# Performance work log

Measured on AMD Instinct MI355X. Metric: run time of the kernel, lower is better.

Reference implementation:

```python
import jax, jax.numpy as jnp
import numpy as np

B, S, H = 8, 2048, 1024
D = H // 16  # head_size = hidden_size // n_heads = 64


def setup_inputs() -> dict:
    key = jax.random.key(0)
    ks = jax.random.split(key, 7)
    scale = 1.0 / np.sqrt(H)
    x = jax.random.normal(ks[0], (B, S, H), dtype=jnp.float32)
    mask = jnp.ones((B, S), dtype=jnp.int32)
    Wq = jax.random.uniform(ks[1], (H, D), jnp.float32, -scale, scale)
    bq = jax.random.uniform(ks[2], (D,), jnp.float32, -scale, scale)
    Wk = jax.random.uniform(ks[3], (H, D), jnp.float32, -scale, scale)
    bk = jax.random.uniform(ks[4], (D,), jnp.float32, -scale, scale)
    Wv = jax.random.uniform(ks[5], (H, D), jnp.float32, -scale, scale)
    bv = jax.random.uniform(ks[6], (D,), jnp.float32, -scale, scale)
    return {"x": x, "mask": mask, "Wq": Wq, "bq": bq, "Wk": Wk, "bk": bk, "Wv": Wv, "bv": bv}


def reference(x, mask, Wq, bq, Wk, bk, Wv, bv):
    # projections: [B,S,H] @ [H,D] -> [B,S,D]
    q = jnp.einsum("bsh,hd->bsd", x, Wq) + bq
    k = jnp.einsum("bsh,hd->bsd", x, Wk) + bk
    v = jnp.einsum("bsh,hd->bsd", x, Wv) + bv
    # scores: [B,S,S]
    scores = jnp.einsum("bqd,bkd->bqk", q, k) / jnp.sqrt(jnp.asarray(q.shape[-1], q.dtype))
    # mask: [B,S] -> [B,1,S]; fill masked keys with -inf
    scores = jnp.where(mask[:, None, :] == 0, -jnp.inf, scores)
    attn = jax.nn.softmax(scores, axis=-1)
    # dropout prob is 0.0 (inference semantics) -> identity
    return jnp.einsum("bqk,bkd->bqd", attn, v)
```

## Files before the change

### kernel.cpp

```cpp
#include <hip/hip_runtime.h>

typedef __bf16 bf16x8 __attribute__((ext_vector_type(8)));
typedef __bf16 bf16x4 __attribute__((ext_vector_type(4)));
typedef float f32x4 __attribute__((ext_vector_type(4)));
typedef float f32x16 __attribute__((ext_vector_type(16)));
typedef unsigned short u16x8 __attribute__((ext_vector_type(8)));

#define MFMA16(a, b, c) __builtin_amdgcn_mfma_f32_16x16x32_bf16((a), (b), (c), 0, 0, 0)
#define MFMA32(a, b, c) __builtin_amdgcn_mfma_f32_32x32x16_bf16((a), (b), (c), 0, 0, 0)

#define SCALE_Q 0.180336880f
#define DEFER_TH 11.5415603f

static __device__ __forceinline__ float fexp2(float x) {
  return __builtin_amdgcn_exp2f(x);
}

static __device__ __forceinline__ unsigned short f2bf(float f) {
  unsigned int u = __float_as_uint(f);
  u += 0x7fffu + ((u >> 16) & 1u);
  return (unsigned short)(u >> 16);
}
static __device__ __forceinline__ float bf2f(unsigned short s) {
  return __uint_as_float((unsigned int)s << 16);
}
static __device__ __forceinline__ unsigned int cvtpk(float lo, float hi) {
  unsigned int r;
  asm("v_cvt_pk_bf16_f32 %0, %1, %2" : "=v"(r) : "v"(lo), "v"(hi));
  return r;
}
static __device__ __forceinline__ void plswap(unsigned int& a, unsigned int& b) {
  asm("v_permlane32_swap_b32 %0, %1" : "+v"(a), "+v"(b));
}

static __device__ __forceinline__ void gld_lds16(const void* g, void* l) {
  __builtin_amdgcn_global_load_lds(
      (const __attribute__((address_space(1))) unsigned int*)(g),
      (__attribute__((address_space(3))) unsigned int*)(l), 16, 0, 0);
}

__global__ __launch_bounds__(128) void wt_kernel(
    const float* __restrict__ Wq, const float* __restrict__ Wk,
    const float* __restrict__ Wv, unsigned short* __restrict__ Wt,
    const int* __restrict__ mask, float* __restrict__ mAddG) {
  const int bid = blockIdx.x;
  if (bid >= 192) {
    const int idx = (bid - 192) * 128 + threadIdx.x;
    mAddG[idx] = mask[idx] ? 0.0f : -__builtin_inff();
    return;
  }
  const int n = bid;
  const int jl = threadIdx.x;
  const float* W;
  int col;
  float scale;
  if (n < 64)       { W = Wq; col = n;       scale = SCALE_Q; }
  else if (n < 128) { W = Wk; col = n - 64;  scale = 1.0f; }
  else              { W = Wv; col = n - 128; scale = 1.0f; }
  const int js = (jl & ~7) | ((jl & 7) ^ (n & 7));
  u16x8 o;
#pragma unroll
  for (int e = 0; e < 8; ++e) o[e] = f2bf(W[(jl * 8 + e) * 64 + col] * scale);
  *reinterpret_cast<u16x8*>(&Wt[n * 1024 + js * 8]) = o;
}

__global__ __launch_bounds__(512, 4) void qkv_kernel(
    const float* __restrict__ x, const unsigned short* __restrict__ Wt,
    const float* __restrict__ bq, const float* __restrict__ bk,
    const float* __restrict__ bv, unsigned short* __restrict__ Q,
    unsigned short* __restrict__ K, unsigned short* __restrict__ Vt) {
  __shared__ __align__(16) unsigned short xs[2][32][72];
  __shared__ __align__(16) unsigned short ws[2][192 * 64];
  const int tid = threadIdx.x;
  const int w = tid >> 6, lane = tid & 63;
  const int lr = lane & 15, lg = lane >> 4;
  const int wg = w >> 2, wc = w & 3;
  const int m0 = blockIdx.x * 32;

  const int xrow = tid >> 4, xc4 = (tid & 15) * 4;
  const float* xsrc = x + (m0 + xrow) * 1024 + xc4;
  const unsigned short* wsrc0 = Wt + ((0 * 512 + tid) >> 3) * 1024 + (tid & 7) * 8;
  const unsigned short* wsrc1 = Wt + ((1 * 512 + tid) >> 3) * 1024 + (tid & 7) * 8;
  const unsigned short* wsrc2 = Wt + ((2 * 512 + tid) >> 3) * 1024 + (tid & 7) * 8;

  f32x4 acc[3] = {};
  const int arow = wg * 16 + lr;

#define WSTAGE(k0, buf)                                                      \
  do {                                                                       \
    gld_lds16(wsrc0 + (k0), (char*)(&ws[buf][0]) + w * 1024);                \
    gld_lds16(wsrc1 + (k0), (char*)(&ws[buf][0]) + 8192 + w * 1024);         \
    gld_lds16(wsrc2 + (k0), (char*)(&ws[buf][0]) + 16384 + w * 1024);        \
  } while (0)
#define XWRITE(v, buf)                                                       \
  do {                                                                       \
    bf16x4 xb;                                                               \
    xb[0] = (__bf16)(v).x; xb[1] = (__bf16)(v).y;                            \
    xb[2] = (__bf16)(v).z; xb[3] = (__bf16)(v).w;                            \
    *reinterpret_cast<bf16x4*>(&xs[buf][xrow][xc4]) = xb;                    \
  } while (0)

  float4 xrA = *reinterpret_cast<const float4*>(xsrc);
  WSTAGE(0, 0);
  XWRITE(xrA, 0);
  xrA = *reinterpret_cast<const float4*>(xsrc + 64);
  asm volatile("s_waitcnt vmcnt(1) lgkmcnt(0)" ::: "memory");
  __builtin_amdgcn_s_barrier();

#pragma unroll
  for (int t = 0; t < 16; ++t) {
    const int cur = t & 1;
    if (t < 15) WSTAGE((t + 1) * 64, cur ^ 1);
    __builtin_amdgcn_sched_barrier(0);
    float4 xrB = {};
    if (t < 14)
      xrB = *reinterpret_cast<const float4*>(xsrc + (t + 2) * 64);
    __builtin_amdgcn_sched_barrier(0);

    bf16x8 a[2];
#pragma unroll
    for (int kh = 0; kh < 2; ++kh)
      a[kh] = *reinterpret_cast<const bf16x8*>(&xs[cur][arow][kh * 32 + lg * 8]);
#pragma unroll
    for (int cf = 0; cf < 3; ++cf) {
      const int n = wc * 48 + cf * 16 + lr;
      const unsigned short* wr = &ws[cur][n * 64];
#pragma unroll
      for (int kh = 0; kh < 2; ++kh) {
        const int sc = (kh * 4 + lg) ^ (n & 7);
        bf16x8 bv8 = *reinterpret_cast<const bf16x8*>(wr + sc * 8);
        acc[cf] = MFMA16(a[kh], bv8, acc[cf]);
      }
    }
    if (t < 15) {
      XWRITE(xrA, cur ^ 1);
      if (t < 14)
        asm volatile("s_waitcnt vmcnt(1) lgkmcnt(0)" ::: "memory");
      else
        asm volatile("s_waitcnt vmcnt(0) lgkmcnt(0)" ::: "memory");
      __builtin_amdgcn_s_barrier();
      xrA = xrB;
    }
  }
#undef WSTAGE
#undef XWRITE

  const int mb = m0 + wg * 16 + lg * 4;
  const int b = m0 >> 11;
#pragma unroll
  for (int cf = 0; cf < 3; ++cf) {
    const int n = wc * 48 + cf * 16 + lr;
    if (n < 64) {
      const float bias = bq[n] * SCALE_Q;
#pragma unroll
      for (int i = 0; i < 4; ++i) Q[(mb + i) * 64 + n] = f2bf(acc[cf][i] + bias);
    } else if (n < 128) {
      const int nn = n - 64;
      const float bias = bk[nn];
#pragma unroll
      for (int i = 0; i < 4; ++i) K[(mb + i) * 64 + nn] = f2bf(acc[cf][i] + bias);
    } else {
      const int d = n - 128;
      const float bias = bv[d];
      ushort4 o;
      o.x = f2bf(acc[cf][0] + bias);
      o.y = f2bf(acc[cf][1] + bias);
      o.z = f2bf(acc[cf][2] + bias);
      o.w = f2bf(acc[cf][3] + bias);
      const int sl = (m0 & 2047) + wg * 16 + lg * 4;
      *reinterpret_cast<ushort4*>(&Vt[((b * 64 + d) << 11) + sl]) = o;
    }
  }
}

__global__ __launch_bounds__(256) void attn_kernel(
    const unsigned short* __restrict__ Q, const unsigned short* __restrict__ K,
    const unsigned short* __restrict__ Vt, const float* __restrict__ mAddG,
    const int* __restrict__ maskI, unsigned short* __restrict__ Opb,
    float* __restrict__ mp, float* __restrict__ lp) {
  __shared__ __align__(16) unsigned short ks[64][72];
  __shared__ __align__(16) unsigned short vs[64][72];
  __shared__ int fl[4];

  const int qt = blockIdx.x, b = blockIdx.y, c = blockIdx.z;
  const int tid = threadIdx.x;
  const int w = tid >> 6, lane = tid & 63;
  const int l31 = lane & 31, h = lane >> 5;
  const int bh = b * 2048;
  const int qb = qt * 128 + w * 32;
  const int sr = tid >> 3, scc = (tid & 7) * 8;

  {
    const int mz = ((maskI[bh + c * 512 + tid] == 0) ? 1 : 0) |
                   ((maskI[bh + c * 512 + 256 + tid] == 0) ? 1 : 0);
    const unsigned long long bal = __ballot(mz);
    if (lane == 0) fl[w] = (bal != 0ull) ? 1 : 0;
  }
  __syncthreads();
  const bool hasMask = (fl[0] | fl[1] | fl[2] | fl[3]) != 0;

  bf16x8 qf[4];
#pragma unroll
  for (int dt = 0; dt < 4; ++dt)
    qf[dt] = *reinterpret_cast<const bf16x8*>(
        &Q[(bh + qb + l31) * 64 + dt * 16 + h * 8]);

  uint4 rk0, rk1, rv0, rv1;
  {
    const int kv0 = c * 512;
    rk0 = *reinterpret_cast<const uint4*>(&K[(bh + kv0 + sr) * 64 + scc]);
    rk1 = *reinterpret_cast<const uint4*>(&K[(bh + kv0 + 32 + sr) * 64 + scc]);
    rv0 = *reinterpret_cast<const uint4*>(&Vt[(b * 64 + sr) * 2048 + kv0 + scc]);
    rv1 = *reinterpret_cast<const uint4*>(&Vt[(b * 64 + 32 + sr) * 2048 + kv0 + scc]);
  }

  f32x16 oacc[2] = {};
  float m_s = -__builtin_inff(), l_s = 0.0f;

  for (int it = 0; it < 8; ++it) {
    const int kv0 = c * 512 + it * 64;
    __builtin_amdgcn_s_barrier();

    *reinterpret_cast<uint4*>(&ks[sr][scc]) = rk0;
    *reinterpret_cast<uint4*>(&ks[32 + sr][scc]) = rk1;
    *reinterpret_cast<uint4*>(&vs[sr][scc]) = rv0;
    *reinterpret_cast<uint4*>(&vs[32 + sr][scc]) = rv1;

    if (it < 7) {
      const int kvn = kv0 + 64;
      rk0 = *reinterpret_cast<const uint4*>(&K[(bh + kvn + sr) * 64 + scc]);
      rk1 = *reinterpret_cast<const uint4*>(&K[(bh + kvn + 32 + sr) * 64 + scc]);
      rv0 = *reinterpret_cast<const uint4*>(&Vt[(b * 64 + sr) * 2048 + kvn + scc]);
      rv1 = *reinterpret_cast<const uint4*>(&Vt[(b * 64 + 32 + sr) * 2048 + kvn + scc]);
    }

    asm volatile("s_waitcnt lgkmcnt(0)" ::: "memory");
    __builtin_amdgcn_s_barrier();

    f32x16 st0 = {}, st1 = {};
    __builtin_amdgcn_s_setprio(1);
#pragma unroll
    for (int dt = 0; dt < 4; ++dt) {
      const bf16x8 kf0 = *reinterpret_cast<const bf16x8*>(&ks[l31][dt * 16 + h * 8]);
      st0 = MFMA32(kf0, qf[dt], st0);
    }
#pragma unroll
    for (int dt = 0; dt < 4; ++dt) {
      const bf16x8 kf1 = *reinterpret_cast<const bf16x8*>(&ks[32 + l31][dt * 16 + h * 8]);
      st1 = MFMA32(kf1, qf[dt], st1);
    }
    __builtin_amdgcn_s_setprio(0);

    if (hasMask) {
#pragma unroll
      for (int rb = 0; rb < 4; ++rb) {
        const f32x4 md0 =
            *reinterpret_cast<const f32x4*>(&mAddG[bh + kv0 + rb * 8 + 4 * h]);
        const f32x4 md1 = *reinterpret_cast<const f32x4*>(
            &mAddG[bh + kv0 + 32 + rb * 8 + 4 * h]);
#pragma unroll
        for (int j = 0; j < 4; ++j) {
          st0[rb * 4 + j] += md0[j];
          st1[rb * 4 + j] += md1[j];
        }
      }
    }

    float pm = st0[0];
#pragma unroll
    for (int r = 1; r < 16; ++r) pm = fmaxf(pm, st0[r]);
#pragma unroll
    for (int r = 0; r < 16; ++r) pm = fmaxf(pm, st1[r]);
    pm = fmaxf(pm, __shfl_xor(pm, 32));
    const float nm = fmaxf(m_s, pm);
    if (!__all(nm <= m_s + DEFER_TH)) {
      const float scn = fexp2(m_s - nm);
      m_s = nm;
      l_s *= scn;
#pragma unroll
      for (int r = 0; r < 16; ++r) {
        const float scr = __shfl(scn, (r & 3) + 8 * (r >> 2) + 4 * h);
        oacc[0][r] *= scr;
        oacc[1][r] *= scr;
      }
    }
    const float mexp = (m_s == -__builtin_inff()) ? 0.0f : m_s;
    float rs = 0.0f;
#pragma unroll
    for (int r = 0; r < 16; ++r) {
      const float p0 = fexp2(st0[r] - mexp);
      st0[r] = p0;
      rs += p0;
      const float p1 = fexp2(st1[r] - mexp);
      st1[r] = p1;
      rs += p1;
    }
    rs += __shfl_xor(rs, 32);
    l_s += rs;

    unsigned int paw[4][4];
#pragma unroll
    for (int kt16 = 0; kt16 < 4; ++kt16) {
      const int lo = kt16 & 1;
      unsigned int X0, X1, Y0, Y1;
      if (kt16 < 2) {
        X0 = cvtpk(st0[lo * 8 + 0], st0[lo * 8 + 1]);
        Y0 = cvtpk(st0[lo * 8 + 2], st0[lo * 8 + 3]);
        X1 = cvtpk(st0[lo * 8 + 4], st0[lo * 8 + 5]);
        Y1 = cvtpk(st0[lo * 8 + 6], st0[lo * 8 + 7]);
      } else {
        X0 = cvtpk(st1[lo * 8 + 0], st1[lo * 8 + 1]);
        Y0 = cvtpk(st1[lo * 8 + 2], st1[lo * 8 + 3]);
        X1 = cvtpk(st1[lo * 8 + 4], st1[lo * 8 + 5]);
        Y1 = cvtpk(st1[lo * 8 + 6], st1[lo * 8 + 7]);
      }
      plswap(X0, X1);
      plswap(Y0, Y1);
      paw[kt16][0] = X0;
      paw[kt16][1] = Y0;
      paw[kt16][2] = X1;
      paw[kt16][3] = Y1;
    }

    __builtin_amdgcn_s_setprio(1);
#pragma unroll
    for (int nf = 0; nf < 2; ++nf)
#pragma unroll
      for (int kt16 = 0; kt16 < 4; ++kt16) {
        const bf16x8 vb = *reinterpret_cast<const bf16x8*>(
            &vs[nf * 32 + l31][kt16 * 16 + h * 8]);
        const bf16x8 pa = *reinterpret_cast<const bf16x8*>(&paw[kt16][0]);
        oacc[nf] = MFMA32(pa, vb, oacc[nf]);
      }
    __builtin_amdgcn_s_setprio(0);
  }

  const float inv_s = (l_s > 0.0f) ? 1.0f / l_s : 0.0f;
#pragma unroll
  for (int r = 0; r < 16; ++r) {
    const int qoff = (r & 3) + 8 * (r >> 2) + 4 * h;
    const float invr = __shfl(inv_s, qoff);
    const int row = bh + qb + qoff;
    Opb[(c * 16384 + row) * 64 + l31] = f2bf(oacc[0][r] * invr);
    Opb[(c * 16384 + row) * 64 + 32 + l31] = f2bf(oacc[1][r] * invr);
  }
  if (h == 0) {
    mp[c * 16384 + bh + qb + l31] = m_s;
    lp[c * 16384 + bh + qb + l31] = l_s;
  }
}

__global__ __launch_bounds__(256) void merge_kernel(
    const unsigned short* __restrict__ Opb, const float* __restrict__ mp,
    const float* __restrict__ lp, float* __restrict__ out) {
  const int t = blockIdx.x * 256 + threadIdx.x;
  const int row = t >> 4;
  const int cc = (t & 15) * 4;
  float mv[4], lv[4];
#pragma unroll
  for (int c = 0; c < 4; ++c) {
    mv[c] = mp[c * 16384 + row];
    lv[c] = lp[c * 16384 + row];
  }
  float M = fmaxf(fmaxf(mv[0], mv[1]), fmaxf(mv[2], mv[3]));
  float L = 0.0f;
  f32x4 o = {};
#pragma unroll
  for (int c = 0; c < 4; ++c) {
    const float wc = __builtin_amdgcn_exp2f(mv[c] - M) * lv[c];
    L += wc;
    const ushort4 u = *reinterpret_cast<const ushort4*>(
        &Opb[(c * 16384 + row) * 64 + cc]);
    f32x4 oc;
    oc[0] = bf2f(u.x); oc[1] = bf2f(u.y); oc[2] = bf2f(u.z); oc[3] = bf2f(u.w);
    o += oc * wc;
  }
  const float inv = 1.0f / L;
  *reinterpret_cast<f32x4*>(&out[row * 64 + cc]) = o * inv;
}

extern "C" void kernel_launch(void* const* d_in, const int* in_sizes, int n_in,
                              void* d_out, int out_size, void* d_ws, size_t ws_size,
                              hipStream_t stream) {
  const float* x  = (const float*)d_in[0];
  const int* mask = (const int*)d_in[1];
  const float* Wq = (const float*)d_in[2];
  const float* bq = (const float*)d_in[3];
  const float* Wk = (const float*)d_in[4];
  const float* bk = (const float*)d_in[5];
  const float* Wv = (const float*)d_in[6];
  const float* bv = (const float*)d_in[7];
  float* out = (float*)d_out;

  unsigned short* Wt = (unsigned short*)d_ws;
  unsigned short* Qw = Wt + 192 * 1024;
  unsigned short* Kw = Qw + 16384 * 64;
  unsigned short* Vt = Kw + 16384 * 64;
  unsigned short* Opb = Vt + 16384 * 64;
  float* mAddG = (float*)(Opb + 4 * 16384 * 64);
  float* mp = mAddG + 16384;
  float* lp = mp + 4 * 16384;

  hipLaunchKernelGGL(wt_kernel, dim3(320), dim3(128), 0, stream,
                     Wq, Wk, Wv, Wt, mask, mAddG);
  hipLaunchKernelGGL(qkv_kernel, dim3(512), dim3(512), 0, stream,
                     x, Wt, bq, bk, bv, Qw, Kw, Vt);
  hipLaunchKernelGGL(attn_kernel, dim3(16, 8, 4), dim3(256), 0, stream,
                     Qw, Kw, Vt, mAddG, mask, Opb, mp, lp);
  hipLaunchKernelGGL(merge_kernel, dim3(1024), dim3(256), 0, stream,
                     Opb, mp, lp, out);
}
```

Before: 47.96 us.

## Double QKV projection M-tile to 64 rows to reuse weight tiles

The QKV projection kernel now processes 64 rows of x per block instead of 32. Each wave computes two 16-row sub-tiles, so every weight fragment read from LDS feeds two MFMAs, and the grid halves to 256 blocks. This cuts redundant weight loads from global memory and LDS per output row. In exchange it uses more accumulators and registers, lowers the occupancy hint to 2, and leaves fewer blocks than CUs on a 256-CU device, which may reduce parallelism.

```diff
diff --git a/kernel.cpp b/kernel.cpp
--- a/kernel.cpp
+++ b/kernel.cpp
@@ -64,18 +64,18 @@
   *reinterpret_cast<u16x8*>(&Wt[n * 1024 + js * 8]) = o;
 }
 
-__global__ __launch_bounds__(512, 4) void qkv_kernel(
+__global__ __launch_bounds__(512, 2) void qkv_kernel(
     const float* __restrict__ x, const unsigned short* __restrict__ Wt,
     const float* __restrict__ bq, const float* __restrict__ bk,
     const float* __restrict__ bv, unsigned short* __restrict__ Q,
     unsigned short* __restrict__ K, unsigned short* __restrict__ Vt) {
-  __shared__ __align__(16) unsigned short xs[2][32][72];
+  __shared__ __align__(16) unsigned short xs[2][64][72];
   __shared__ __align__(16) unsigned short ws[2][192 * 64];
   const int tid = threadIdx.x;
   const int w = tid >> 6, lane = tid & 63;
   const int lr = lane & 15, lg = lane >> 4;
   const int wg = w >> 2, wc = w & 3;
-  const int m0 = blockIdx.x * 32;
+  const int m0 = blockIdx.x * 64;
 
   const int xrow = tid >> 4, xc4 = (tid & 15) * 4;
   const float* xsrc = x + (m0 + xrow) * 1024 + xc4;
@@ -83,8 +83,8 @@
   const unsigned short* wsrc1 = Wt + ((1 * 512 + tid) >> 3) * 1024 + (tid & 7) * 8;
   const unsigned short* wsrc2 = Wt + ((2 * 512 + tid) >> 3) * 1024 + (tid & 7) * 8;
 
-  f32x4 acc[3] = {};
-  const int arow = wg * 16 + lr;
+  f32x4 acc[2][3] = {};
+  const int arow = wg * 32 + lr;
 
 #define WSTAGE(k0, buf)                                                      \
   do {                                                                       \
@@ -92,19 +92,24 @@
     gld_lds16(wsrc1 + (k0), (char*)(&ws[buf][0]) + 8192 + w * 1024);         \
     gld_lds16(wsrc2 + (k0), (char*)(&ws[buf][0]) + 16384 + w * 1024);        \
   } while (0)
-#define XWRITE(v, buf)                                                       \
+#define XWRITE(v0, v1, buf)                                                  \
   do {                                                                       \
-    bf16x4 xb;                                                               \
-    xb[0] = (__bf16)(v).x; xb[1] = (__bf16)(v).y;                            \
-    xb[2] = (__bf16)(v).z; xb[3] = (__bf16)(v).w;                            \
-    *reinterpret_cast<bf16x4*>(&xs[buf][xrow][xc4]) = xb;                    \
+    bf16x4 t0, t1;                                                           \
+    t0[0] = (__bf16)(v0).x; t0[1] = (__bf16)(v0).y;                          \
+    t0[2] = (__bf16)(v0).z; t0[3] = (__bf16)(v0).w;                          \
+    t1[0] = (__bf16)(v1).x; t1[1] = (__bf16)(v1).y;                          \
+    t1[2] = (__bf16)(v1).z; t1[3] = (__bf16)(v1).w;                          \
+    *reinterpret_cast<bf16x4*>(&xs[buf][xrow][xc4]) = t0;                    \
+    *reinterpret_cast<bf16x4*>(&xs[buf][xrow + 32][xc4]) = t1;               \
   } while (0)
 
-  float4 xrA = *reinterpret_cast<const float4*>(xsrc);
+  float4 xrA0 = *reinterpret_cast<const float4*>(xsrc);
+  float4 xrA1 = *reinterpret_cast<const float4*>(xsrc + 32 * 1024);
   WSTAGE(0, 0);
-  XWRITE(xrA, 0);
-  xrA = *reinterpret_cast<const float4*>(xsrc + 64);
-  asm volatile("s_waitcnt vmcnt(1) lgkmcnt(0)" ::: "memory");
+  XWRITE(xrA0, xrA1, 0);
+  xrA0 = *reinterpret_cast<const float4*>(xsrc + 64);
+  xrA1 = *reinterpret_cast<const float4*>(xsrc + 32 * 1024 + 64);
+  asm volatile("s_waitcnt vmcnt(2) lgkmcnt(0)" ::: "memory");
   __builtin_amdgcn_s_barrier();
 
 #pragma unroll
@@ -112,15 +117,20 @@
     const int cur = t & 1;
     if (t < 15) WSTAGE((t + 1) * 64, cur ^ 1);
     __builtin_amdgcn_sched_barrier(0);
-    float4 xrB = {};
-    if (t < 14)
-      xrB = *reinterpret_cast<const float4*>(xsrc + (t + 2) * 64);
+    float4 xrB0 = {}, xrB1 = {};
+    if (t < 14) {
+      xrB0 = *reinterpret_cast<const float4*>(xsrc + (t + 2) * 64);
+      xrB1 = *reinterpret_cast<const float4*>(xsrc + 32 * 1024 + (t + 2) * 64);
+    }
     __builtin_amdgcn_sched_barrier(0);
 
-    bf16x8 a[2];
-#pragma unroll
-    for (int kh = 0; kh < 2; ++kh)
-      a[kh] = *reinterpret_cast<const bf16x8*>(&xs[cur][arow][kh * 32 + lg * 8]);
+    bf16x8 a[2][2];
+#pragma unroll
+    for (int sub = 0; sub < 2; ++sub)
+#pragma unroll
+      for (int kh = 0; kh < 2; ++kh)
+        a[sub][kh] = *reinterpret_cast<const bf16x8*>(
+            &xs[cur][arow + sub * 16][kh * 32 + lg * 8]);
 #pragma unroll
     for (int cf = 0; cf < 3; ++cf) {
       const int n = wc * 48 + cf * 16 + lr;
@@ -128,47 +138,54 @@
 #pragma unroll
       for (int kh = 0; kh < 2; ++kh) {
         const int sc = (kh * 4 + lg) ^ (n & 7);
-        bf16x8 bv8 = *reinterpret_cast<const bf16x8*>(wr + sc * 8);
-        acc[cf] = MFMA16(a[kh], bv8, acc[cf]);
+        const bf16x8 bv8 = *reinterpret_cast<const bf16x8*>(wr + sc * 8);
+        acc[0][cf] = MFMA16(a[0][kh], bv8, acc[0][cf]);
+        acc[1][cf] = MFMA16(a[1][kh], bv8, acc[1][cf]);
       }
     }
     if (t < 15) {
-      XWRITE(xrA, cur ^ 1);
+      XWRITE(xrA0, xrA1, cur ^ 1);
       if (t < 14)
-        asm volatile("s_waitcnt vmcnt(1) lgkmcnt(0)" ::: "memory");
+        asm volatile("s_waitcnt vmcnt(2) lgkmcnt(0)" ::: "memory");
       else
         asm volatile("s_waitcnt vmcnt(0) lgkmcnt(0)" ::: "memory");
       __builtin_amdgcn_s_barrier();
-      xrA = xrB;
+      xrA0 = xrB0;
+      xrA1 = xrB1;
     }
   }
 #undef WSTAGE
 #undef XWRITE
 
-  const int mb = m0 + wg * 16 + lg * 4;
   const int b = m0 >> 11;
 #pragma unroll
-  for (int cf = 0; cf < 3; ++cf) {
-    const int n = wc * 48 + cf * 16 + lr;
-    if (n < 64) {
-      const float bias = bq[n] * SCALE_Q;
-#pragma unroll
-      for (int i = 0; i < 4; ++i) Q[(mb + i) * 64 + n] = f2bf(acc[cf][i] + bias);
-    } else if (n < 128) {
-      const int nn = n - 64;
-      const float bias = bk[nn];
-#pragma unroll
-      for (int i = 0; i < 4; ++i) K[(mb + i) * 64 + nn] = f2bf(acc[cf][i] + bias);
-    } else {
-      const int d = n - 128;
-      const float bias = bv[d];
-      ushort4 o;
-      o.x = f2bf(acc[cf][0] + bias);
-      o.y = f2bf(acc[cf][1] + bias);
-      o.z = f2bf(acc[cf][2] + bias);
-      o.w = f2bf(acc[cf][3] + bias);
-      const int sl = (m0 & 2047) + wg * 16 + lg * 4;
-      *reinterpret_cast<ushort4*>(&Vt[((b * 64 + d) << 11) + sl]) = o;
+  for (int sub = 0; sub < 2; ++sub) {
+    const int mb = m0 + wg * 32 + sub * 16 + lg * 4;
+#pragma unroll
+    for (int cf = 0; cf < 3; ++cf) {
+      const int n = wc * 48 + cf * 16 + lr;
+      if (n < 64) {
+        const float bias = bq[n] * SCALE_Q;
+#pragma unroll
+        for (int i = 0; i < 4; ++i)
+          Q[(mb + i) * 64 + n] = f2bf(acc[sub][cf][i] + bias);
+      } else if (n < 128) {
+        const int nn = n - 64;
+        const float bias = bk[nn];
+#pragma unroll
+        for (int i = 0; i < 4; ++i)
+          K[(mb + i) * 64 + nn] = f2bf(acc[sub][cf][i] + bias);
+      } else {
+        const int d = n - 128;
+        const float bias = bv[d];
+        ushort4 o;
+        o.x = f2bf(acc[sub][cf][0] + bias);
+        o.y = f2bf(acc[sub][cf][1] + bias);
+        o.z = f2bf(acc[sub][cf][2] + bias);
+        o.w = f2bf(acc[sub][cf][3] + bias);
+        const int sl = (m0 & 2047) + wg * 32 + sub * 16 + lg * 4;
+        *reinterpret_cast<ushort4*>(&Vt[((b * 64 + d) << 11) + sl]) = o;
+      }
     }
   }
 }
@@ -403,7 +420,7 @@
 
   hipLaunchKernelGGL(wt_kernel, dim3(320), dim3(128), 0, stream,
                      Wq, Wk, Wv, Wt, mask, mAddG);
-  hipLaunchKernelGGL(qkv_kernel, dim3(512), dim3(512), 0, stream,
+  hipLaunchKernelGGL(qkv_kernel, dim3(256), dim3(512), 0, stream,
                      x, Wt, bq, bk, bv, Qw, Kw, Vt);
   hipLaunchKernelGGL(attn_kernel, dim3(16, 8, 4), dim3(256), 0, stream,
                      Qw, Kw, Vt, mAddG, mask, Opb, mp, lp);
```

New measurement: 50.36 us. 1.05x slower.
